# Performance work log

Measured on AMD Instinct MI355X. Metric: run time of the kernel, lower is better.

## Reference

```python
import jax, jax.numpy as jnp
import numpy as np


def setup_inputs() -> dict:
    key = jax.random.key(0)
    heatmaps = jax.random.normal(key, (16, 24, 64, 64, 64), dtype=jnp.float32)
    return {"heatmaps": heatmaps}


def reference(heatmaps):
    N, J, D, H, W = heatmaps.shape
    # Softmax over the flattened D*H*W volume (the intended normalization).
    p = jax.nn.softmax(heatmaps.reshape(N, J, D * H * W), axis=-1)
    p = p.reshape(N, J, D, H, W)
    # Axis marginals: sum out the other two spatial axes.
    x_maps = p.sum(axis=(2, 3))  # [N, J, W]
    y_maps = p.sum(axis=(2, 4))  # [N, J, H]
    z_maps = p.sum(axis=(3, 4))  # [N, J, D]
    # Soft-argmax expectation, normalized to roughly [-0.5, 0.5).
    x_preds = (x_maps * jnp.arange(W, dtype=p.dtype)).sum(axis=2) / W - 0.5
    y_preds = (y_maps * jnp.arange(H, dtype=p.dtype)).sum(axis=2) / H - 0.5
    z_preds = (z_maps * jnp.arange(D, dtype=p.dtype)).sum(axis=2) / D - 0.5
    return jnp.stack((x_preds, y_preds, z_preds), axis=2)  # [N, J, 3]
```

## Files before the change

kernel.cpp:

```cpp
#include <hip/hip_runtime.h>
#include <math.h>


#define SLABS       384
#define SLAB_ELEMS  262144
#define CHUNKS      4
#define BLOCK       256
#define CHUNK_ELEMS (SLAB_ELEMS / CHUNKS)
#define ITERS       (CHUNK_ELEMS / (BLOCK * 4))

__device__ __forceinline__ float fast_exp2(float x) {
#if __has_builtin(__builtin_amdgcn_exp2f)
    return __builtin_amdgcn_exp2f(x);
#else
    return exp2f(x);
#endif
}

__device__ __forceinline__ void combine(float& ml, float& S, float& Sx, float& Sy, float& Sz,
                                        float oml, float oS, float oSx, float oSy, float oSz) {
    float nml = fmaxf(ml, oml);
    float sa = fast_exp2(ml - nml);
    float sb = fast_exp2(oml - nml);
    S  = S * sa  + oS * sb;
    Sx = Sx * sa + oSx * sb;
    Sy = Sy * sa + oSy * sb;
    Sz = Sz * sa + oSz * sb;
    ml = nml;
}

__global__ __launch_bounds__(BLOCK) void jir_partial_kernel(const float* __restrict__ in,
                                                            float* __restrict__ ws) {
    const int slab  = blockIdx.x / CHUNKS;
    const int chunk = blockIdx.x % CHUNKS;
    const float* base = in + (size_t)slab * SLAB_ELEMS + (size_t)chunk * CHUNK_ELEMS;
    const int tid = threadIdx.x;

    const float LOG2E = 1.4426950408889634f;

    float ml = -INFINITY;
    float S = 0.f, Sx = 0.f, Sy = 0.f, Sz = 0.f;

    const int idx0 = chunk * CHUNK_ELEMS;

#pragma unroll 4
    for (int it = 0; it < ITERS; ++it) {
        const int vi = it * BLOCK + tid;
        const float4 v = ((const float4*)base)[vi];
        const int idx = idx0 + vi * 4;
        const float w0 = (float)(idx & 63);
        const float hh = (float)((idx >> 6) & 63);
        const float dd = (float)(idx >> 12);

        const float vmax = fmaxf(fmaxf(v.x, v.y), fmaxf(v.z, v.w));
        const float nml = vmax * LOG2E;
        if (nml > ml) {
            const float scale = fast_exp2(ml - nml);
            S *= scale; Sx *= scale; Sy *= scale; Sz *= scale;
            ml = nml;
        }
        const float e0 = fast_exp2(__builtin_fmaf(v.x, LOG2E, -ml));
        const float e1 = fast_exp2(__builtin_fmaf(v.y, LOG2E, -ml));
        const float e2 = fast_exp2(__builtin_fmaf(v.z, LOG2E, -ml));
        const float e3 = fast_exp2(__builtin_fmaf(v.w, LOG2E, -ml));
        const float s = (e0 + e1) + (e2 + e3);
        S  += s;
        Sx += s * w0 + (e1 + 2.f * e2 + 3.f * e3);
        Sy += s * hh;
        Sz += s * dd;
    }

#pragma unroll
    for (int off = 1; off < 64; off <<= 1) {
        float oml = __shfl_xor(ml, off, 64);
        float oS  = __shfl_xor(S,  off, 64);
        float oSx = __shfl_xor(Sx, off, 64);
        float oSy = __shfl_xor(Sy, off, 64);
        float oSz = __shfl_xor(Sz, off, 64);
        combine(ml, S, Sx, Sy, Sz, oml, oS, oSx, oSy, oSz);
    }

    __shared__ float red[4][5];
    const int wave = tid >> 6;
    const int lane = tid & 63;
    if (lane == 0) {
        red[wave][0] = ml; red[wave][1] = S; red[wave][2] = Sx;
        red[wave][3] = Sy; red[wave][4] = Sz;
    }
    __syncthreads();
    if (tid == 0) {
        float fml = red[0][0], fS = red[0][1], fSx = red[0][2], fSy = red[0][3], fSz = red[0][4];
#pragma unroll
        for (int wv = 1; wv < 4; ++wv) {
            combine(fml, fS, fSx, fSy, fSz,
                    red[wv][0], red[wv][1], red[wv][2], red[wv][3], red[wv][4]);
        }
        float* o = ws + (size_t)blockIdx.x * 5;
        o[0] = fml; o[1] = fS; o[2] = fSx; o[3] = fSy; o[4] = fSz;
    }
}

__global__ __launch_bounds__(64) void jir_finalize_kernel(const float* __restrict__ ws,
                                                          float* __restrict__ out) {
    const int slab = blockIdx.x * 64 + threadIdx.x;
    if (slab >= SLABS) return;

    const float* p0 = ws + (size_t)slab * CHUNKS * 5;
    float ml = p0[0], S = p0[1], Sx = p0[2], Sy = p0[3], Sz = p0[4];
#pragma unroll
    for (int c = 1; c < CHUNKS; ++c) {
        const float* p = p0 + c * 5;
        combine(ml, S, Sx, Sy, Sz, p[0], p[1], p[2], p[3], p[4]);
    }
    const float inv = 1.0f / S;
    out[slab * 3 + 0] = (Sx * inv) * (1.0f / 64.0f) - 0.5f;
    out[slab * 3 + 1] = (Sy * inv) * (1.0f / 64.0f) - 0.5f;
    out[slab * 3 + 2] = (Sz * inv) * (1.0f / 64.0f) - 0.5f;
}

extern "C" void kernel_launch(void* const* d_in, const int* in_sizes, int n_in,
                              void* d_out, int out_size, void* d_ws, size_t ws_size,
                              hipStream_t stream) {
    const float* heatmaps = (const float*)d_in[0];
    float* out = (float*)d_out;
    float* ws = (float*)d_ws;

    jir_partial_kernel<<<SLABS * CHUNKS, BLOCK, 0, stream>>>(heatmaps, ws);
    jir_finalize_kernel<<<(SLABS + 63) / 64, 64, 0, stream>>>(ws, out);
}
```

Measured before the change: 515.6 us.

## Double chunks, software-pipeline nontemporal loads, hoist index math out of loop

```diff
diff --git a/kernel.cpp b/kernel.cpp
--- a/kernel.cpp
+++ b/kernel.cpp
@@ -4,10 +4,13 @@
 
 #define SLABS       384
 #define SLAB_ELEMS  262144
-#define CHUNKS      4
+#define CHUNKS      8
 #define BLOCK       256
 #define CHUNK_ELEMS (SLAB_ELEMS / CHUNKS)
-#define ITERS       (CHUNK_ELEMS / (BLOCK * 4))
+#define CHUNK_VEC4  (CHUNK_ELEMS / 4)
+#define ITERS       (CHUNK_VEC4 / (BLOCK * 2))
+
+typedef float f32x4 __attribute__((ext_vector_type(4)));
 
 __device__ __forceinline__ float fast_exp2(float x) {
 #if __has_builtin(__builtin_amdgcn_exp2f)
@@ -33,41 +36,63 @@
                                                             float* __restrict__ ws) {
     const int slab  = blockIdx.x / CHUNKS;
     const int chunk = blockIdx.x % CHUNKS;
-    const float* base = in + (size_t)slab * SLAB_ELEMS + (size_t)chunk * CHUNK_ELEMS;
+    const f32x4* __restrict__ B =
+        (const f32x4*)(in + (size_t)slab * SLAB_ELEMS + (size_t)chunk * CHUNK_ELEMS);
     const int tid = threadIdx.x;
 
     const float LOG2E = 1.4426950408889634f;
 
+    const float w0f   = (float)((4 * tid) & 63);
+    const float hbase = (float)(tid >> 4);
+    const float dbase = (float)(chunk * 8);
+
     float ml = -INFINITY;
     float S = 0.f, Sx = 0.f, Sy = 0.f, Sz = 0.f;
 
-    const int idx0 = chunk * CHUNK_ELEMS;
+    f32x4 va = __builtin_nontemporal_load(B + tid);
+    f32x4 vb = __builtin_nontemporal_load(B + tid + BLOCK);
 
-#pragma unroll 4
+#pragma unroll
     for (int it = 0; it < ITERS; ++it) {
-        const int vi = it * BLOCK + tid;
-        const float4 v = ((const float4*)base)[vi];
-        const int idx = idx0 + vi * 4;
-        const float w0 = (float)(idx & 63);
-        const float hh = (float)((idx >> 6) & 63);
-        const float dd = (float)(idx >> 12);
+        f32x4 na, nb;
+        if (it < ITERS - 1) {
+            na = __builtin_nontemporal_load(B + (it + 1) * (2 * BLOCK) + tid);
+            nb = __builtin_nontemporal_load(B + (it + 1) * (2 * BLOCK) + tid + BLOCK);
+        }
 
-        const float vmax = fmaxf(fmaxf(v.x, v.y), fmaxf(v.z, v.w));
-        const float nml = vmax * LOG2E;
+        const float h0f = hbase + (float)((it & 1) << 5);
+        const float ddf = dbase + (float)(it >> 1);
+
+        const float mA = fmaxf(fmaxf(va.x, va.y), fmaxf(va.z, va.w));
+        const float mB = fmaxf(fmaxf(vb.x, vb.y), fmaxf(vb.z, vb.w));
+        const float nml = fmaxf(mA, mB) * LOG2E;
         if (nml > ml) {
             const float scale = fast_exp2(ml - nml);
             S *= scale; Sx *= scale; Sy *= scale; Sz *= scale;
             ml = nml;
         }
-        const float e0 = fast_exp2(__builtin_fmaf(v.x, LOG2E, -ml));
-        const float e1 = fast_exp2(__builtin_fmaf(v.y, LOG2E, -ml));
-        const float e2 = fast_exp2(__builtin_fmaf(v.z, LOG2E, -ml));
-        const float e3 = fast_exp2(__builtin_fmaf(v.w, LOG2E, -ml));
-        const float s = (e0 + e1) + (e2 + e3);
-        S  += s;
-        Sx += s * w0 + (e1 + 2.f * e2 + 3.f * e3);
-        Sy += s * hh;
-        Sz += s * dd;
+
+        const float a0 = fast_exp2(__builtin_fmaf(va.x, LOG2E, -ml));
+        const float a1 = fast_exp2(__builtin_fmaf(va.y, LOG2E, -ml));
+        const float a2 = fast_exp2(__builtin_fmaf(va.z, LOG2E, -ml));
+        const float a3 = fast_exp2(__builtin_fmaf(va.w, LOG2E, -ml));
+        const float b0 = fast_exp2(__builtin_fmaf(vb.x, LOG2E, -ml));
+        const float b1 = fast_exp2(__builtin_fmaf(vb.y, LOG2E, -ml));
+        const float b2 = fast_exp2(__builtin_fmaf(vb.z, LOG2E, -ml));
+        const float b3 = fast_exp2(__builtin_fmaf(vb.w, LOG2E, -ml));
+
+        const float sA = (a0 + a1) + (a2 + a3);
+        const float sB = (b0 + b1) + (b2 + b3);
+        const float xA = __builtin_fmaf(3.f, a3, __builtin_fmaf(2.f, a2, a1));
+        const float xB = __builtin_fmaf(3.f, b3, __builtin_fmaf(2.f, b2, b1));
+        const float sAB = sA + sB;
+
+        S  += sAB;
+        Sx  = __builtin_fmaf(sAB, w0f, Sx + (xA + xB));
+        Sy  = __builtin_fmaf(sAB, h0f, __builtin_fmaf(16.f, sB, Sy));
+        Sz  = __builtin_fmaf(sAB, ddf, Sz);
+
+        va = na; vb = nb;
     }
 
 #pragma unroll
```

After: 481.7 us. 6.6% less time.

## Double-buffer four float4 loads per iteration with nontemporal loads and hoisted index math

Applied to the files above, without the earlier changes.

```diff
diff --git a/kernel.cpp b/kernel.cpp
--- a/kernel.cpp
+++ b/kernel.cpp
@@ -4,10 +4,12 @@
 
 #define SLABS       384
 #define SLAB_ELEMS  262144
-#define CHUNKS      4
+#define CHUNKS      8
 #define BLOCK       256
 #define CHUNK_ELEMS (SLAB_ELEMS / CHUNKS)
-#define ITERS       (CHUNK_ELEMS / (BLOCK * 4))
+#define ITERS       (CHUNK_ELEMS / (BLOCK * 16))
+
+typedef float f32x4 __attribute__((ext_vector_type(4)));
 
 __device__ __forceinline__ float fast_exp2(float x) {
 #if __has_builtin(__builtin_amdgcn_exp2f)
@@ -29,45 +31,79 @@
     ml = nml;
 }
 
+__device__ __forceinline__ float max4(f32x4 v) {
+    return fmaxf(fmaxf(v.x, v.y), fmaxf(v.z, v.w));
+}
+
+__device__ __forceinline__ void pack_exp(f32x4 v, float ml, float& s, float& x) {
+    const float LOG2E = 1.4426950408889634f;
+    const float e0 = fast_exp2(__builtin_fmaf(v.x, LOG2E, -ml));
+    const float e1 = fast_exp2(__builtin_fmaf(v.y, LOG2E, -ml));
+    const float e2 = fast_exp2(__builtin_fmaf(v.z, LOG2E, -ml));
+    const float e3 = fast_exp2(__builtin_fmaf(v.w, LOG2E, -ml));
+    s = (e0 + e1) + (e2 + e3);
+    x = __builtin_fmaf(3.f, e3, __builtin_fmaf(2.f, e2, e1));
+}
+
 __global__ __launch_bounds__(BLOCK) void jir_partial_kernel(const float* __restrict__ in,
                                                             float* __restrict__ ws) {
     const int slab  = blockIdx.x / CHUNKS;
     const int chunk = blockIdx.x % CHUNKS;
-    const float* base = in + (size_t)slab * SLAB_ELEMS + (size_t)chunk * CHUNK_ELEMS;
+    const f32x4* __restrict__ B =
+        (const f32x4*)(in + (size_t)slab * SLAB_ELEMS + (size_t)chunk * CHUNK_ELEMS);
     const int tid = threadIdx.x;
 
     const float LOG2E = 1.4426950408889634f;
 
+    const float w0f   = (float)((4 * tid) & 63);
+    const float h0f   = (float)(tid >> 4);
+    const float dbase = (float)(chunk * 8);
+
     float ml = -INFINITY;
     float S = 0.f, Sx = 0.f, Sy = 0.f, Sz = 0.f;
 
-    const int idx0 = chunk * CHUNK_ELEMS;
+    f32x4 c0 = __builtin_nontemporal_load(B + tid);
+    f32x4 c1 = __builtin_nontemporal_load(B + tid + 256);
+    f32x4 c2 = __builtin_nontemporal_load(B + tid + 512);
+    f32x4 c3 = __builtin_nontemporal_load(B + tid + 768);
 
-#pragma unroll 4
+#pragma unroll
     for (int it = 0; it < ITERS; ++it) {
-        const int vi = it * BLOCK + tid;
-        const float4 v = ((const float4*)base)[vi];
-        const int idx = idx0 + vi * 4;
-        const float w0 = (float)(idx & 63);
-        const float hh = (float)((idx >> 6) & 63);
-        const float dd = (float)(idx >> 12);
+        f32x4 n0, n1, n2, n3;
+        if (it < ITERS - 1) {
+            const int nb = (it + 1) * 1024 + tid;
+            n0 = __builtin_nontemporal_load(B + nb);
+            n1 = __builtin_nontemporal_load(B + nb + 256);
+            n2 = __builtin_nontemporal_load(B + nb + 512);
+            n3 = __builtin_nontemporal_load(B + nb + 768);
+        }
 
-        const float vmax = fmaxf(fmaxf(v.x, v.y), fmaxf(v.z, v.w));
-        const float nml = vmax * LOG2E;
+        const float ddf = dbase + (float)it;
+
+        const float nml = fmaxf(fmaxf(max4(c0), max4(c1)),
+                                fmaxf(max4(c2), max4(c3))) * LOG2E;
         if (nml > ml) {
             const float scale = fast_exp2(ml - nml);
             S *= scale; Sx *= scale; Sy *= scale; Sz *= scale;
             ml = nml;
         }
-        const float e0 = fast_exp2(__builtin_fmaf(v.x, LOG2E, -ml));
-        const float e1 = fast_exp2(__builtin_fmaf(v.y, LOG2E, -ml));
-        const float e2 = fast_exp2(__builtin_fmaf(v.z, LOG2E, -ml));
-        const float e3 = fast_exp2(__builtin_fmaf(v.w, LOG2E, -ml));
-        const float s = (e0 + e1) + (e2 + e3);
-        S  += s;
-        Sx += s * w0 + (e1 + 2.f * e2 + 3.f * e3);
-        Sy += s * hh;
-        Sz += s * dd;
+
+        float s0, s1, s2, s3, x0, x1, x2, x3;
+        pack_exp(c0, ml, s0, x0);
+        pack_exp(c1, ml, s1, x1);
+        pack_exp(c2, ml, s2, x2);
+        pack_exp(c3, ml, s3, x3);
+
+        const float s_tot = (s0 + s1) + (s2 + s3);
+        const float xsum  = (x0 + x1) + (x2 + x3);
+        const float hq    = __builtin_fmaf(3.f, s3, __builtin_fmaf(2.f, s2, s1));
+
+        S  += s_tot;
+        Sx  = __builtin_fmaf(s_tot, w0f, Sx + xsum);
+        Sy  = __builtin_fmaf(s_tot, h0f, __builtin_fmaf(16.f, hq, Sy));
+        Sz  = __builtin_fmaf(s_tot, ddf, Sz);
+
+        c0 = n0; c1 = n1; c2 = n2; c3 = n3;
     }
 
 #pragma unroll
```

Result: faster. 483.2 us (-6.3%).
